# Performance work log

Hardware: AMD Instinct MI355X
Metric: run time of the kernel (lower is better)

The kernel has to match this reference:

```python
import jax, jax.numpy as jnp
import numpy as np

NUM_EDGE = 5
NUM_CHANNELS = 2
NUM_NODES = 2048
W_IN = 256
W_OUT = 128
NUM_CLASS = 16
NUM_LAYERS = 2


def gtconv(A, w):
    """Softmax-weighted mix of edge-type adjacencies.
    A: [E, N, N], w: [E, C] -> [C, N, N].
    Equivalent to concatenating COO edge lists scaled by filter[j, i] and
    summing duplicates (what the scipy round-trip does implicitly)."""
    f = jax.nn.softmax(w, axis=0)  # softmax over edge types (dim=0)
    return jnp.einsum('enm,ec->cnm', A, f)


def degree_normalize(H):
    """GTN.normalization: deg = scatter_add over col, value *= deg[col]^-1 (col scaling).
    H: [C, N, N]; deg over rows (axis=1) gives per-column in-degree."""
    deg = H.sum(axis=1)  # [C, N]
    dinv = jnp.where(deg > 0, 1.0 / jnp.where(deg > 0, deg, 1.0), 0.0)
    return H * dinv[:, None, :]


def setup_inputs() -> dict:
    key = jax.random.key(0)
    ks = jax.random.split(key, 8)
    A = jax.random.uniform(ks[0], (NUM_EDGE, NUM_NODES, NUM_NODES), dtype=jnp.float32)
    h = jax.random.normal(ks[1], (NUM_NODES, W_IN), dtype=jnp.float32)
    # GTConv weights: init std=0.01 as in reset_parameters
    w1 = jax.random.normal(ks[2], (NUM_EDGE, NUM_CHANNELS), dtype=jnp.float32) * 0.01
    w2 = jax.random.normal(ks[3], (NUM_EDGE, NUM_CHANNELS), dtype=jnp.float32) * 0.01
    w_layers = jax.random.normal(ks[4], (NUM_LAYERS - 1, NUM_EDGE, NUM_CHANNELS), dtype=jnp.float32) * 0.01
    gcn_w = jax.random.normal(ks[5], (W_IN, W_OUT), dtype=jnp.float32) * (1.0 / np.sqrt(W_IN))
    gcn_b = jnp.zeros((W_OUT,), dtype=jnp.float32)
    lin1_w = jax.random.normal(ks[6], (W_OUT * NUM_CHANNELS, W_OUT), dtype=jnp.float32) * (1.0 / np.sqrt(W_OUT * NUM_CHANNELS))
    lin1_b = jnp.zeros((W_OUT,), dtype=jnp.float32)
    lin2_w = jax.random.normal(ks[7], (W_OUT, NUM_CLASS), dtype=jnp.float32) * (1.0 / np.sqrt(W_OUT))
    lin2_b = jnp.zeros((NUM_CLASS,), dtype=jnp.float32)
    return {"A": A, "h": h, "w1": w1, "w2": w2, "w_layers": w_layers,
            "gcn_w": gcn_w, "gcn_b": gcn_b, "lin1_w": lin1_w, "lin1_b": lin1_b,
            "lin2_w": lin2_w, "lin2_b": lin2_b}


def reference(A, h, w1, w2, w_layers, gcn_w, gcn_b, lin1_w, lin1_b, lin2_w, lin2_b):
    # Layer 0 (first=True): H[c] = conv1(A)[c] @ conv2(A)[c], then degree norm.
    H = jnp.einsum('cnk,ckm->cnm', gtconv(A, w1), gtconv(A, w2))
    H = degree_normalize(H)
    # Layers 1..L-1 (first=False): H[c] = H[c] @ conv(A)[c], then degree norm.
    for i in range(w_layers.shape[0]):
        B = gtconv(A, w_layers[i])
        H = jnp.einsum('cnk,ckm->cnm', H, B)
        H = degree_normalize(H)
    # Shared GCN per channel (DGL GraphConv, norm='both'): weight first (w_in > w_out),
    # src out-degree^-1/2 scaling, aggregate along edges src->dst, dst in-degree^-1/2.
    hw = h @ gcn_w                                   # [N, w_out]
    dout = jnp.clip(H.sum(axis=2), 1.0, None) ** -0.5  # [C, N] src norm
    din = jnp.clip(H.sum(axis=1), 1.0, None) ** -0.5   # [C, N] dst norm
    agg = jnp.einsum('cnm,cnd->cmd', H, dout[:, :, None] * hw[None])  # dst m gathers from src n
    X = jax.nn.relu(agg * din[:, :, None] + gcn_b)   # [C, N, w_out]
    # Concatenate channels along feature dim (channel-major, matching th.cat order)
    X = jnp.transpose(X, (1, 0, 2)).reshape(H.shape[1], -1)  # [N, C*w_out]
    X = jax.nn.relu(X @ lin1_w + lin1_b)
    return X @ lin2_w + lin2_b
```

## Files before the change

### kernel.cpp

```cpp
#include <hip/hip_runtime.h>

typedef unsigned short u16;
typedef __attribute__((ext_vector_type(4))) float f32x4;
typedef __attribute__((ext_vector_type(8))) __bf16 bf16x8;
typedef __attribute__((ext_vector_type(8))) unsigned short us8;

#define NN (2048ull*2048ull)


__device__ __forceinline__ u16 f2b(float x){
  union { float f; unsigned u; } v; v.f = x;
  unsigned r = v.u + 0x7FFFu + ((v.u >> 16) & 1u);
  return (u16)(r >> 16);
}
__device__ __forceinline__ float b2f(u16 x){
  union { unsigned u; float f; } v; v.u = ((unsigned)x) << 16; return v.f;
}

__global__ __launch_bounds__(256)
void k_zero(float4* __restrict__ p, int n4){
  const float4 z = {0.f,0.f,0.f,0.f};
  for (int i = blockIdx.x*256 + threadIdx.x; i < n4; i += gridDim.x*256)
    p[i] = z;
}

__global__ __launch_bounds__(256)
void k_mix(const float* __restrict__ A,
           const float* __restrict__ w1, const float* __restrict__ w2,
           const float* __restrict__ wl,
           u16* __restrict__ A1T, u16* __restrict__ A2T, u16* __restrict__ BT,
           float* __restrict__ sA1, float* __restrict__ deg2){
  __shared__ float stg[2][16*256];
  const int t = threadIdx.x;
  const int mt = blockIdx.x;
  const int nt = blockIdx.y;
  const int m0 = mt*256, n0 = nt*16;

  float f[3][2][5];
  #pragma unroll
  for (int s=0;s<3;s++){
    const float* w = (s==0) ? w1 : (s==1) ? w2 : wl;
    #pragma unroll
    for (int c=0;c<2;c++){
      float m = -1e30f;
      #pragma unroll
      for (int e=0;e<5;e++) m = fmaxf(m, w[e*2+c]);
      float sum = 0.f;
      #pragma unroll
      for (int e=0;e<5;e++){ f[s][c][e] = __expf(w[e*2+c]-m); sum += f[s][c][e]; }
      float inv = 1.f/sum;
      #pragma unroll
      for (int e=0;e<5;e++) f[s][c][e] *= inv;
    }
  }

  float acc[6][16];
  #pragma unroll
  for (int sc=0;sc<6;sc++)
    #pragma unroll
    for (int n=0;n<16;n++) acc[sc][n] = 0.f;

  auto stage = [&](int buf, int e){
    #pragma unroll
    for (int it=0; it<4; ++it)
      __builtin_amdgcn_global_load_lds(
        (const __attribute__((address_space(1))) void*)
          (A + (size_t)e*NN + (size_t)(n0 + it*4 + (t>>6))*2048 + m0 + (t&63)*4),
        (__attribute__((address_space(3))) void*)(&stg[buf][it*1024 + t*4]), 16, 0, 0);
  };

  stage(0, 0);
  #pragma unroll
  for (int e=0; e<5; ++e){
    const int cur = e & 1;
    if (e < 4) stage(cur ^ 1, e + 1);
    if (e < 4) asm volatile("s_waitcnt vmcnt(4)" ::: "memory");
    else       asm volatile("s_waitcnt vmcnt(0)" ::: "memory");
    __builtin_amdgcn_sched_barrier(0);
    __builtin_amdgcn_s_barrier();
    __builtin_amdgcn_sched_barrier(0);
    #pragma unroll
    for (int n=0;n<16;n++){
      float a = stg[cur][n*256 + t];
      #pragma unroll
      for (int s=0;s<3;s++)
        #pragma unroll
        for (int c=0;c<2;c++)
          acc[s*2+c][n] += a * f[s][c][e];
    }
    __builtin_amdgcn_s_barrier();
    __builtin_amdgcn_sched_barrier(0);
  }

  #pragma unroll
  for (int c=0;c<2;c++){
    float p1 = 0.f, pB = 0.f;
    #pragma unroll
    for (int n=0;n<16;n++){ p1 += acc[0+c][n]; pB += acc[4+c][n]; }
    atomicAdd(&sA1[c*2048 + m0 + t], p1);
    atomicAdd(&deg2[c*2048 + m0 + t], pB);
  }
  const size_t tb = (size_t)(nt*8 + mt)*4096 + (size_t)t*16;
  #pragma unroll
  for (int sc=0; sc<6; ++sc){
    u16* __restrict__ dst = (sc<2) ? A1T : (sc<4) ? A2T : BT;
    const int c = sc & 1;
    us8 v0, v1;
    #pragma unroll
    for (int q=0;q<8;q++){ v0[q] = f2b(acc[sc][q]); v1[q] = f2b(acc[sc][8+q]); }
    *(us8*)&dst[(size_t)c*NN + tb]     = v0;
    *(us8*)&dst[(size_t)c*NN + tb + 8] = v1;
  }
}

__global__ __launch_bounds__(256)
void k_rdot(const u16* __restrict__ A2T, const float* __restrict__ sA1,
            float* __restrict__ deg1){
  const int mt = blockIdx.x, ng = blockIdx.y, c = blockIdx.z;
  const int t = threadIdx.x;
  const u16* __restrict__ Mc = A2T + (size_t)c*NN;
  const float* __restrict__ sv = sA1 + c*2048;
  float s = 0.f;
  #pragma unroll 2
  for (int q=0; q<16; ++q){
    const int ntile = ng*16 + q;
    const u16* base = Mc + (size_t)(ntile*8 + mt)*4096 + (size_t)t*16;
    us8 v0 = *(const us8*)base;
    us8 v1 = *(const us8*)(base + 8);
    const float4 f0 = *(const float4*)&sv[ntile*16 + 0];
    const float4 f1 = *(const float4*)&sv[ntile*16 + 4];
    const float4 f2 = *(const float4*)&sv[ntile*16 + 8];
    const float4 f3 = *(const float4*)&sv[ntile*16 + 12];
    s += b2f(v0[0])*f0.x + b2f(v0[1])*f0.y + b2f(v0[2])*f0.z + b2f(v0[3])*f0.w
       + b2f(v0[4])*f1.x + b2f(v0[5])*f1.y + b2f(v0[6])*f1.z + b2f(v0[7])*f1.w
       + b2f(v1[0])*f2.x + b2f(v1[1])*f2.y + b2f(v1[2])*f2.z + b2f(v1[3])*f2.w
       + b2f(v1[4])*f3.x + b2f(v1[5])*f3.y + b2f(v1[6])*f3.z + b2f(v1[7])*f3.w;
  }
  atomicAdd(&deg1[c*2048 + mt*256 + t], s);
}

template<int MODE>
__global__ __launch_bounds__(256)
void k_wsum(const u16* __restrict__ MT, const float* __restrict__ va,
            const float* __restrict__ vb, float* __restrict__ outv){
  __shared__ float w[512];
  __shared__ float red[16][17];
  const int t = threadIdx.x;
  const int nt = blockIdx.x, mgrp = blockIdx.y, c = blockIdx.z;
  #pragma unroll
  for (int i=t; i<512; i+=256){
    const int m = c*2048 + mgrp*512 + i;
    float x;
    if (MODE == 0){ float d = va[m]; x = d > 0.f ? 1.f/d : 0.f; }
    else if (MODE == 1){ float d = va[m]; x = (d > 0.f ? 1.f/d : 0.f) * vb[m]; }
    else { x = va[m]; }
    w[i] = x;
  }
  __syncthreads();
  const int n = t & 15, mg = t >> 4;
  float s = 0.f;
  #pragma unroll
  for (int mt2=0; mt2<2; ++mt2){
    const u16* __restrict__ base = MT + (size_t)c*NN
        + (size_t)(nt*8 + mgrp*2 + mt2)*4096 + n;
    #pragma unroll 4
    for (int mm=0; mm<16; ++mm){
      const int ml = mg*16 + mm;
      s += b2f(base[ml*16]) * w[mt2*256 + ml];
    }
  }
  red[mg][n] = s;
  __syncthreads();
  if (t < 16){
    float sum = 0.f;
    #pragma unroll
    for (int g=0; g<16; ++g) sum += red[g][t];
    atomicAdd(&outv[c*2048 + nt*16 + t], sum);
  }
}

__global__ __launch_bounds__(256)
void k_hwpt(const float* __restrict__ h, const float* __restrict__ W,
            const float* __restrict__ rowsum, u16* __restrict__ PT){
  __shared__ float lh[8][256];
  int t = threadIdx.x;
  int n0 = blockIdx.x * 8;
  for (int idx = t; idx < 8*256; idx += 256)
    lh[idx >> 8][idx & 255] = h[(size_t)(n0 + (idx>>8))*256 + (idx&255)];
  __syncthreads();
  int d = t & 127, half = t >> 7;
  float acc[4];
  #pragma unroll
  for (int nn=0;nn<4;nn++) acc[nn] = 0.f;
  for (int k=0;k<256;k++){
    float wv = W[(size_t)k*128 + d];
    #pragma unroll
    for (int nn=0;nn<4;nn++) acc[nn] += lh[half*4+nn][k]*wv;
  }
  #pragma unroll
  for (int c=0;c<2;c++){
    ushort4 o;
    #pragma unroll
    for (int nn=0;nn<4;nn++){
      int n = n0 + half*4 + nn;
      float dv = rsqrtf(fmaxf(rowsum[c*2048 + n], 1.0f));
      ((u16*)&o)[nn] = f2b(dv * acc[nn]);
    }
    *(ushort4*)&PT[((size_t)c*128 + d)*2048 + n0 + half*4] = o;
  }
}

__global__ __launch_bounds__(256, 2)
void k_gemm3(const u16* __restrict__ A, const u16* __restrict__ Bt, float* __restrict__ Agg){
  __shared__ u16 lA[128*64];
  __shared__ u16 lB[128*64];
  const int tid = threadIdx.x;
  const int bm = blockIdx.x, bk = blockIdx.y, cc = blockIdx.z;
  const u16* __restrict__ Bb = Bt + (size_t)cc*(128*2048) + bk*256;
  float* __restrict__ Cb = Agg + (size_t)cc*2048*128 + (size_t)(bm*128)*128;
  const int wid = tid >> 6, lane = tid & 63;
  const int wr = wid >> 1, wc = wid & 1;
  const int fl = lane & 15, fk = (lane >> 4) << 3;
  const int srow = (wid << 3) + (lane >> 3);
  const int scol = (lane & 7) << 3;

  f32x4 acc[4][4];
  const f32x4 zero = {0.f,0.f,0.f,0.f};
  #pragma unroll
  for (int i=0;i<4;i++)
    #pragma unroll
    for (int jj=0;jj<4;jj++) acc[i][jj] = zero;

  for (int k0 = 0; k0 < 256; k0 += 64){
    #pragma unroll
    for (int it = 0; it < 4; ++it){
      const int m = bm*128 + it*32 + srow;
      const int n = bk*256 + k0 + scol;
      const u16* srcA = A + (size_t)cc*NN
          + (size_t)((n>>4)*8 + (m>>8))*4096 + (size_t)(m&255)*16 + (n&15);
      __builtin_amdgcn_global_load_lds(
        (const __attribute__((address_space(1))) void*)srcA,
        (__attribute__((address_space(3))) void*)(&lA[(it*32 + (wid<<3))*64]), 16, 0, 0);
      int r = it*32 + srow;
      __builtin_amdgcn_global_load_lds(
        (const __attribute__((address_space(1))) void*)(Bb + (size_t)r*2048 + k0 + scol),
        (__attribute__((address_space(3))) void*)(&lB[(it*32 + (wid<<3))*64]), 16, 0, 0);
    }
    __syncthreads();
    #pragma unroll
    for (int ks = 0; ks < 2; ++ks){
      bf16x8 af[4], bfr[4];
      #pragma unroll
      for (int mi=0;mi<4;mi++)
        af[mi] = *reinterpret_cast<const bf16x8*>(&lA[(wr*64 + mi*16 + fl)*64 + ks*32 + fk]);
      #pragma unroll
      for (int ni=0;ni<4;ni++)
        bfr[ni] = *reinterpret_cast<const bf16x8*>(&lB[(wc*64 + ni*16 + fl)*64 + ks*32 + fk]);
      #pragma unroll
      for (int mi=0;mi<4;mi++)
        #pragma unroll
        for (int ni=0;ni<4;ni++)
          acc[mi][ni] = __builtin_amdgcn_mfma_f32_16x16x32_bf16(af[mi], bfr[ni], acc[mi][ni], 0, 0, 0);
    }
    __syncthreads();
  }
  const int rbase = (lane >> 4) << 2;
  #pragma unroll
  for (int mi=0;mi<4;mi++)
    #pragma unroll
    for (int ni=0;ni<4;ni++)
      #pragma unroll
      for (int r=0;r<4;r++)
        atomicAdd(&Cb[(size_t)(wr*64 + mi*16 + rbase + r)*128 + wc*64 + ni*16 + fl],
                  acc[mi][ni][r]);
}

template<bool SCALE>
__global__ __launch_bounds__(256)
void k_qt(const float* __restrict__ Agg, const float* __restrict__ deg1,
          u16* __restrict__ QT){
  __shared__ u16 lq[128][36];
  const int t = threadIdx.x;
  const int m0 = blockIdx.x * 32, c = blockIdx.y;
  const int d4 = (t & 31) * 4, mr = t >> 5;
  #pragma unroll
  for (int p4=0; p4<4; ++p4){
    const int m = m0 + p4*8 + mr;
    float4 s = *(const float4*)&Agg[((size_t)c*2048 + m)*128 + d4];
    if (SCALE){
      float dg = deg1[c*2048 + m];
      float di = dg > 0.f ? 1.f/dg : 0.f;
      s.x *= di; s.y *= di; s.z *= di; s.w *= di;
    }
    const int ml = p4*8 + mr;
    lq[d4+0][ml] = f2b(s.x); lq[d4+1][ml] = f2b(s.y);
    lq[d4+2][ml] = f2b(s.z); lq[d4+3][ml] = f2b(s.w);
  }
  __syncthreads();
  const int d = t >> 1, half = t & 1;
  u16* __restrict__ dst = QT + ((size_t)c*128 + d)*2048 + m0 + half*16;
  #pragma unroll
  for (int q=0;q<4;q++){
    ushort4 o;
    o.x = lq[d][half*16 + q*4 + 0];
    o.y = lq[d][half*16 + q*4 + 1];
    o.z = lq[d][half*16 + q*4 + 2];
    o.w = lq[d][half*16 + q*4 + 3];
    *(ushort4*)&dst[q*4] = o;
  }
}

__global__ __launch_bounds__(256)
void k_head(const float* __restrict__ agg3, const float* __restrict__ deg2,
            const float* __restrict__ gb,
            const float* __restrict__ W1, const float* __restrict__ b1,
            const float* __restrict__ W2, const float* __restrict__ b2,
            float* __restrict__ out){
  __shared__ float lx[8][256];
  __shared__ float lt[8][132];
  int t = threadIdx.x;
  int n0 = blockIdx.x * 8;
  for (int idx = t; idx < 512; idx += 256){
    int row = idx >> 6;
    int q = idx & 63;
    int c = q >> 5, d4 = (q & 31) * 4;
    float dg = deg2[c*2048 + n0 + row];
    float di = dg > 0.f ? 1.f/dg : 0.f;
    float4 s = *(const float4*)&agg3[((size_t)c*2048 + n0 + row)*128 + d4];
    const float4 bv = *(const float4*)&gb[d4];
    s.x = fmaxf(s.x*di + bv.x, 0.f); s.y = fmaxf(s.y*di + bv.y, 0.f);
    s.z = fmaxf(s.z*di + bv.z, 0.f); s.w = fmaxf(s.w*di + bv.w, 0.f);
    *(float4*)&lx[row][c*128 + d4] = s;
  }
  __syncthreads();
  int d = t & 127, half = t >> 7;
  float acc[4];
  #pragma unroll
  for (int nn=0;nn<4;nn++) acc[nn] = 0.f;
  for (int k=0;k<256;k++){
    float wv = W1[(size_t)k*128 + d];
    #pragma unroll
    for (int nn=0;nn<4;nn++) acc[nn] += lx[half*4+nn][k]*wv;
  }
  float bb = b1[d];
  #pragma unroll
  for (int nn=0;nn<4;nn++){
    float v = acc[nn] + bb;
    lt[half*4+nn][d] = v > 0.f ? v : 0.f;
  }
  __syncthreads();
  if (t < 128){
    int row = t >> 4, q = t & 15;
    float s = b2[q];
    for (int dd=0; dd<128; dd++) s += lt[row][dd] * W2[(size_t)dd*16 + q];
    out[(size_t)(n0+row)*16 + q] = s;
  }
}

extern "C" void kernel_launch(void* const* d_in, const int* in_sizes, int n_in,
                              void* d_out, int out_size, void* d_ws, size_t ws_size,
                              hipStream_t stream){
  const float* A   = (const float*)d_in[0];
  const float* h   = (const float*)d_in[1];
  const float* w1  = (const float*)d_in[2];
  const float* w2  = (const float*)d_in[3];
  const float* wl  = (const float*)d_in[4];
  const float* gw  = (const float*)d_in[5];
  const float* gb  = (const float*)d_in[6];
  const float* l1w = (const float*)d_in[7];
  const float* l1b = (const float*)d_in[8];
  const float* l2w = (const float*)d_in[9];
  const float* l2b = (const float*)d_in[10];
  float* out = (float*)d_out;
  char* ws = (char*)d_ws;

  const size_t SZ = 2*NN*2;
  const size_t AGG = (size_t)2*2048*128*4;
  u16*  A1T  = (u16*)(ws);
  u16*  A2T  = (u16*)(ws + 1*SZ);
  u16*  BT   = (u16*)(ws + 2*SZ);
  char* tail = ws + 3*SZ;
  u16*  PT     = (u16*)tail;
  u16*  Q1T    = (u16*)(tail + 1048576);
  u16*  Q2T    = (u16*)(tail + 2*1048576);
  float* sA1   = (float*)(tail + 3*1048576);
  float* deg1  = sA1 + 4096;
  float* deg2  = deg1 + 4096;
  float* v1    = deg2 + 4096;
  float* v3    = v1 + 4096;
  float* rowsum= v3 + 4096;
  float* agg1  = rowsum + 4096;
  float* agg2  = agg1 + 2*2048*128;
  float* agg3  = agg2 + 2*2048*128;
  const size_t ZBYTES = 6*4096*4 + 3*AGG;

  const size_t TOTAL = 3*SZ + 3*1048576 + ZBYTES;
  if (ws_size < TOTAL){ hipMemsetAsync(d_out, 0, (size_t)out_size*4, stream); return; }

  k_zero<<<1024, 256, 0, stream>>>((float4*)sA1, (int)(ZBYTES/16));

  k_mix<<<dim3(8,128), 256, 0, stream>>>(A, w1, w2, wl, A1T, A2T, BT, sA1, deg2);
  k_rdot<<<dim3(8,8,2), 256, 0, stream>>>(A2T, sA1, deg1);
  k_wsum<0><<<dim3(128,4,2), 256, 0, stream>>>(BT, deg2, deg2, v1);
  k_wsum<1><<<dim3(128,4,2), 256, 0, stream>>>(A2T, deg1, v1, v3);
  k_wsum<2><<<dim3(128,4,2), 256, 0, stream>>>(A1T, v3, v3, rowsum);
  k_hwpt<<<256, 256, 0, stream>>>(h, gw, rowsum, PT);
  k_gemm3<<<dim3(16,8,2), 256, 0, stream>>>(A1T, PT, agg1);
  k_qt<false><<<dim3(64,2), 256, 0, stream>>>(agg1, deg1, Q1T);
  k_gemm3<<<dim3(16,8,2), 256, 0, stream>>>(A2T, Q1T, agg2);
  k_qt<true><<<dim3(64,2), 256, 0, stream>>>(agg2, deg1, Q2T);
  k_gemm3<<<dim3(16,8,2), 256, 0, stream>>>(BT, Q2T, agg3);
  k_head<<<256, 256, 0, stream>>>(agg3, deg2, gb, l1w, l1b, l2w, l2b, out);
}
```

Measured before the change: 151.1 us.

## Merge rdot and first wsum into one launch; load GEMM B fragments directly

Combines two independent post-mix kernels (the row-dot for deg1 and the BT weighted column sum for v1) into a single launch, with block ranges picking the role. This saves one launch and lets the two workloads run side by side on the GPU. Separately, the aggregation GEMM stops staging its B operand through LDS and reads the bf16 fragments straight from global memory. That halves LDS use but makes each wave issue uncoalesced global loads inside the MFMA loop.

```diff
diff --git a/kernel.cpp b/kernel.cpp
--- a/kernel.cpp
+++ b/kernel.cpp
@@ -114,29 +114,64 @@
 }
 
 __global__ __launch_bounds__(256)
-void k_rdot(const u16* __restrict__ A2T, const float* __restrict__ sA1,
-            float* __restrict__ deg1){
-  const int mt = blockIdx.x, ng = blockIdx.y, c = blockIdx.z;
+void k_post1(const u16* __restrict__ A2T, const u16* __restrict__ BT,
+             const float* __restrict__ sA1, const float* __restrict__ deg2,
+             float* __restrict__ deg1, float* __restrict__ v1){
+  const int b = blockIdx.x;
   const int t = threadIdx.x;
-  const u16* __restrict__ Mc = A2T + (size_t)c*NN;
-  const float* __restrict__ sv = sA1 + c*2048;
-  float s = 0.f;
-  #pragma unroll 2
-  for (int q=0; q<16; ++q){
-    const int ntile = ng*16 + q;
-    const u16* base = Mc + (size_t)(ntile*8 + mt)*4096 + (size_t)t*16;
-    us8 v0 = *(const us8*)base;
-    us8 v1 = *(const us8*)(base + 8);
-    const float4 f0 = *(const float4*)&sv[ntile*16 + 0];
-    const float4 f1 = *(const float4*)&sv[ntile*16 + 4];
-    const float4 f2 = *(const float4*)&sv[ntile*16 + 8];
-    const float4 f3 = *(const float4*)&sv[ntile*16 + 12];
-    s += b2f(v0[0])*f0.x + b2f(v0[1])*f0.y + b2f(v0[2])*f0.z + b2f(v0[3])*f0.w
-       + b2f(v0[4])*f1.x + b2f(v0[5])*f1.y + b2f(v0[6])*f1.z + b2f(v0[7])*f1.w
-       + b2f(v1[0])*f2.x + b2f(v1[1])*f2.y + b2f(v1[2])*f2.z + b2f(v1[3])*f2.w
-       + b2f(v1[4])*f3.x + b2f(v1[5])*f3.y + b2f(v1[6])*f3.z + b2f(v1[7])*f3.w;
-  }
-  atomicAdd(&deg1[c*2048 + mt*256 + t], s);
+  if (b < 128){
+    const int mt = b & 7, ng = (b >> 3) & 7, c = b >> 6;
+    const u16* __restrict__ Mc = A2T + (size_t)c*NN;
+    const float* __restrict__ sv = sA1 + c*2048;
+    float s = 0.f;
+    #pragma unroll 2
+    for (int q=0; q<16; ++q){
+      const int ntile = ng*16 + q;
+      const u16* base = Mc + (size_t)(ntile*8 + mt)*4096 + (size_t)t*16;
+      us8 v0 = *(const us8*)base;
+      us8 v1r = *(const us8*)(base + 8);
+      const float4 f0 = *(const float4*)&sv[ntile*16 + 0];
+      const float4 f1 = *(const float4*)&sv[ntile*16 + 4];
+      const float4 f2 = *(const float4*)&sv[ntile*16 + 8];
+      const float4 f3 = *(const float4*)&sv[ntile*16 + 12];
+      s += b2f(v0[0])*f0.x + b2f(v0[1])*f0.y + b2f(v0[2])*f0.z + b2f(v0[3])*f0.w
+         + b2f(v0[4])*f1.x + b2f(v0[5])*f1.y + b2f(v0[6])*f1.z + b2f(v0[7])*f1.w
+         + b2f(v1r[0])*f2.x + b2f(v1r[1])*f2.y + b2f(v1r[2])*f2.z + b2f(v1r[3])*f2.w
+         + b2f(v1r[4])*f3.x + b2f(v1r[5])*f3.y + b2f(v1r[6])*f3.z + b2f(v1r[7])*f3.w;
+    }
+    atomicAdd(&deg1[c*2048 + mt*256 + t], s);
+  } else {
+    __shared__ float w[512];
+    __shared__ float red[16][17];
+    const int idx = b - 128;
+    const int nt = idx & 127, mgrp = (idx >> 7) & 3, c = idx >> 9;
+    #pragma unroll
+    for (int i=t; i<512; i+=256){
+      float d = deg2[c*2048 + mgrp*512 + i];
+      w[i] = d > 0.f ? 1.f/d : 0.f;
+    }
+    __syncthreads();
+    const int n = t & 15, mg = t >> 4;
+    float s = 0.f;
+    #pragma unroll
+    for (int mt2=0; mt2<2; ++mt2){
+      const u16* __restrict__ base = BT + (size_t)c*NN
+          + (size_t)(nt*8 + mgrp*2 + mt2)*4096 + n;
+      #pragma unroll 4
+      for (int mm=0; mm<16; ++mm){
+        const int ml = mg*16 + mm;
+        s += b2f(base[ml*16]) * w[mt2*256 + ml];
+      }
+    }
+    red[mg][n] = s;
+    __syncthreads();
+    if (t < 16){
+      float sum = 0.f;
+      #pragma unroll
+      for (int g=0; g<16; ++g) sum += red[g][t];
+      atomicAdd(&v1[c*2048 + nt*16 + t], sum);
+    }
+  }
 }
 
 template<int MODE>
@@ -151,8 +186,7 @@
   for (int i=t; i<512; i+=256){
     const int m = c*2048 + mgrp*512 + i;
     float x;
-    if (MODE == 0){ float d = va[m]; x = d > 0.f ? 1.f/d : 0.f; }
-    else if (MODE == 1){ float d = va[m]; x = (d > 0.f ? 1.f/d : 0.f) * vb[m]; }
+    if (MODE == 1){ float d = va[m]; x = (d > 0.f ? 1.f/d : 0.f) * vb[m]; }
     else { x = va[m]; }
     w[i] = x;
   }
@@ -213,7 +247,6 @@
 __global__ __launch_bounds__(256, 2)
 void k_gemm3(const u16* __restrict__ A, const u16* __restrict__ Bt, float* __restrict__ Agg){
   __shared__ u16 lA[128*64];
-  __shared__ u16 lB[128*64];
   const int tid = threadIdx.x;
   const int bm = blockIdx.x, bk = blockIdx.y, cc = blockIdx.z;
   const u16* __restrict__ Bb = Bt + (size_t)cc*(128*2048) + bk*256;
@@ -241,10 +274,6 @@
       __builtin_amdgcn_global_load_lds(
         (const __attribute__((address_space(1))) void*)srcA,
         (__attribute__((address_space(3))) void*)(&lA[(it*32 + (wid<<3))*64]), 16, 0, 0);
-      int r = it*32 + srow;
-      __builtin_amdgcn_global_load_lds(
-        (const __attribute__((address_space(1))) void*)(Bb + (size_t)r*2048 + k0 + scol),
-        (__attribute__((address_space(3))) void*)(&lB[(it*32 + (wid<<3))*64]), 16, 0, 0);
     }
     __syncthreads();
     #pragma unroll
@@ -255,7 +284,8 @@
         af[mi] = *reinterpret_cast<const bf16x8*>(&lA[(wr*64 + mi*16 + fl)*64 + ks*32 + fk]);
       #pragma unroll
       for (int ni=0;ni<4;ni++)
-        bfr[ni] = *reinterpret_cast<const bf16x8*>(&lB[(wc*64 + ni*16 + fl)*64 + ks*32 + fk]);
+        bfr[ni] = *reinterpret_cast<const bf16x8*>(
+            &Bb[(size_t)(wc*64 + ni*16 + fl)*2048 + k0 + ks*32 + fk]);
       #pragma unroll
       for (int mi=0;mi<4;mi++)
         #pragma unroll
@@ -400,8 +430,7 @@
   k_zero<<<1024, 256, 0, stream>>>((float4*)sA1, (int)(ZBYTES/16));
 
   k_mix<<<dim3(8,128), 256, 0, stream>>>(A, w1, w2, wl, A1T, A2T, BT, sA1, deg2);
-  k_rdot<<<dim3(8,8,2), 256, 0, stream>>>(A2T, sA1, deg1);
-  k_wsum<0><<<dim3(128,4,2), 256, 0, stream>>>(BT, deg2, deg2, v1);
+  k_post1<<<1152, 256, 0, stream>>>(A2T, BT, sA1, deg2, deg1, v1);
   k_wsum<1><<<dim3(128,4,2), 256, 0, stream>>>(A2T, deg1, v1, v3);
   k_wsum<2><<<dim3(128,4,2), 256, 0, stream>>>(A1T, v3, v3, rowsum);
   k_hwpt<<<256, 256, 0, stream>>>(h, gw, rowsum, PT);
```

After: 150.0 us. Within noise of the previous version (-0.8%).
